# Kernel optimization log

Measured on AMD Instinct MI355X. Metric: run time of the kernel, lower is better.

The kernel has to match this reference:

```python
import jax, jax.numpy as jnp
import numpy as np
from jax import lax

L, B, N_IN, N_OUT, K = 1024, 16, 1024, 512, 5


def setup_inputs() -> dict:
    key = jax.random.key(0)
    k0, k1, k2, k3, k4 = jax.random.split(key, 5)
    val_range = (6.0 / (N_IN + N_OUT)) ** 0.5
    x = jax.random.normal(k0, (L, B, N_IN), dtype=jnp.float32)
    weight = jax.random.uniform(k1, (N_IN, N_OUT * K), dtype=jnp.float32,
                                minval=-val_range, maxval=val_range)
    bias = jax.random.normal(k2, (N_OUT * K,), dtype=jnp.float32) * 0.1
    bias_eps = jax.random.normal(k3, (N_OUT,), dtype=jnp.float32) * 0.1
    bias_final = jax.random.normal(k4, (N_OUT * 2,), dtype=jnp.float32) * 0.1
    return {"x": x, "weight": weight, "bias": bias,
            "bias_eps": bias_eps, "bias_final": bias_final}


def reference(x, weight, bias, bias_eps, bias_final):
    # x: [L, B, n_in]; unidirectional (bidir=1), real semiring, output gate, tanh
    length, batch, n_in = x.shape
    n_out = N_OUT
    u_ = (x.reshape(-1, n_in) @ weight).reshape(length, batch, n_out, K)
    b = bias.reshape(K, n_out)  # [5, n_out]: in1, in2, f1, f2, out
    forget_bias1, forget_bias2, output_bias = b[2], b[3], b[4]
    output = jax.nn.sigmoid(u_[..., 4] + output_bias)      # [L, B, n_out]
    forget1 = jax.nn.sigmoid(u_[..., 2] + forget_bias1)
    forget2 = jax.nn.sigmoid(u_[..., 3] + forget_bias2)
    u1, u2 = u_[..., 0], u_[..., 1]
    eps = jax.nn.sigmoid(bias_eps)                          # [n_out]

    def step(carry, inp):
        c1_prev, c2_prev = carry
        f1t, f2t, u1t, u2t = inp
        c1_t = c1_prev * f1t + u1t
        c2_t = c2_prev * f2t + (eps + c1_prev) * u2t
        return (c1_t, c2_t), (c1_t, c2_t)

    init = (jnp.zeros((batch, n_out), x.dtype), jnp.zeros((batch, n_out), x.dtype))
    (c1_final, c2_final), (c1s, c2s) = lax.scan(step, init, (forget1, forget2, u1, u2))

    rho = jax.nn.sigmoid(bias_final.reshape(n_out, 2)) * 2.0
    cs = c1s * rho[:, 0] + c2s * rho[:, 1]
    gcs = jnp.tanh(output * cs)                             # [L, B, n_out]
    return gcs, c1_final, c2_final
```

## Files before the change

kernel.cpp:

```cpp
#include <hip/hip_runtime.h>
#include <cstdint>

#define LSEQ 1024
#define BATCH 16
#define NIN 1024
#define NOUT 512
#define KGATE 5
#define NCOL (NOUT * KGATE)
#define MTOT (LSEQ * BATCH)
#define CHAINS (BATCH * NOUT)
#define OUT_GCS (LSEQ * BATCH * NOUT)
#define SEG 32
#define SLEN 32
#define PLANE ((size_t)MTOT * NOUT)
#define SMP ((size_t)SEG * CHAINS)

typedef _Float16 f16x8 __attribute__((ext_vector_type(8)));
typedef float f32x4 __attribute__((ext_vector_type(4)));

__device__ __forceinline__ void async16(const void* g, void* l) {
    __builtin_amdgcn_global_load_lds(
        (const __attribute__((address_space(1))) void*)(uintptr_t)g,
        (__attribute__((address_space(3))) void*)(uintptr_t)l,
        16, 0, 0);
}

__device__ __forceinline__ float fsigmoid(float x) {
    return 1.0f / (1.0f + __expf(-x));
}

__global__ void convert_x_k(const float* __restrict__ x, _Float16* __restrict__ xb, int n8) {
    int i = blockIdx.x * blockDim.x + threadIdx.x;
    if (i < n8) {
        float4 a = ((const float4*)x)[2 * i];
        float4 b = ((const float4*)x)[2 * i + 1];
        f16x8 h;
        h[0] = (_Float16)a.x; h[1] = (_Float16)a.y; h[2] = (_Float16)a.z; h[3] = (_Float16)a.w;
        h[4] = (_Float16)b.x; h[5] = (_Float16)b.y; h[6] = (_Float16)b.z; h[7] = (_Float16)b.w;
        ((f16x8*)xb)[i] = h;
    }
}

__global__ __launch_bounds__(256) void transpose_w_k(const float* __restrict__ w, _Float16* __restrict__ wT) {
    __shared__ float lds[32][33];
    int t = threadIdx.x;
    int col = t & 31;
    int rowg = t >> 5;
    int n0 = blockIdx.x * 32;
    int k0 = blockIdx.y * 32;
#pragma unroll
    for (int i = 0; i < 4; i++) {
        int r = rowg + i * 8;
        lds[r][col] = w[(size_t)(k0 + r) * NCOL + n0 + col];
    }
    __syncthreads();
#pragma unroll
    for (int i = 0; i < 4; i++) {
        int r = rowg + i * 8;
        int c = n0 + r;
        int row = (c % 5) * NOUT + (c / 5);
        wT[(size_t)row * NIN + k0 + col] = (_Float16)lds[col][r];
    }
}

__global__ __launch_bounds__(256, 2) void gemm_gates_k(const _Float16* __restrict__ A,
                                                       const _Float16* __restrict__ BT,
                                                       const float* __restrict__ bias,
                                                       _Float16* __restrict__ planes) {
    __shared__ _Float16 Al[256 * 64];
    __shared__ _Float16 Bl[128 * 64];
    int t = threadIdx.x;
    int w = t >> 6, lane = t & 63;
    int m0 = blockIdx.x * 256, n0 = blockIdx.y * 128;

    f32x4 acc[8][4] = {};

    const int q = lane >> 4, r16 = lane & 15;
    const int wm = (w >> 1) * 128, wn = (w & 1) * 64;

    for (int kk = 0; kk < NIN; kk += 64) {
#pragma unroll
        for (int cc = 0; cc < 8; cc++) {
            int c = t + cc * 256;
            int r = c >> 3, sg = c & 7;
            async16(A + (size_t)(m0 + r) * NIN + kk + sg * 8, (char*)Al + c * 16);
        }
#pragma unroll
        for (int cc = 0; cc < 4; cc++) {
            int c = t + cc * 256;
            int r = c >> 3, sg = c & 7;
            async16(BT + (size_t)(n0 + r) * NIN + kk + sg * 8, (char*)Bl + c * 16);
        }
        __syncthreads();

#pragma unroll
        for (int h = 0; h < 2; h++) {
            f16x8 af[8], bf[4];
#pragma unroll
            for (int i = 0; i < 8; i++)
                af[i] = *(const f16x8*)(Al + (wm + i * 16 + r16) * 64 + h * 32 + q * 8);
#pragma unroll
            for (int j = 0; j < 4; j++)
                bf[j] = *(const f16x8*)(Bl + (wn + j * 16 + r16) * 64 + h * 32 + q * 8);
#pragma unroll
            for (int i = 0; i < 8; i++)
#pragma unroll
                for (int j = 0; j < 4; j++)
                    acc[i][j] = __builtin_amdgcn_mfma_f32_16x16x32_f16(af[i], bf[j], acc[i][j], 0, 0, 0);
        }
        __syncthreads();
    }

    int g = n0 >> 9;
    int nb = n0 & (NOUT - 1);
    _Float16* plane = planes + (size_t)g * PLANE;
#pragma unroll
    for (int j = 0; j < 4; j++) {
        int coln = nb + wn + j * 16 + r16;
        float bv = bias[n0 + wn + j * 16 + r16];
#pragma unroll
        for (int i = 0; i < 8; i++) {
#pragma unroll
            for (int reg = 0; reg < 4; reg++) {
                int m = m0 + wm + i * 16 + q * 4 + reg;
                float v = acc[i][j][reg];
                if (g >= 2) v = fsigmoid(v + bv);
                plane[(size_t)m * NOUT + coln] = (_Float16)v;
            }
        }
    }
}

__global__ __launch_bounds__(256) void compose_k(const _Float16* __restrict__ planes,
                                                 const float* __restrict__ beps,
                                                 float* __restrict__ SM) {
    int u = blockIdx.x * 256 + threadIdx.x;
    int t = u & (CHAINS - 1);
    int s = u >> 13;
    int n = t & (NOUT - 1);
    float eps = fsigmoid(beps[n]);
    float a11 = 1.0f, a21 = 0.0f, a22 = 1.0f, b1 = 0.0f, b2 = 0.0f;
#pragma unroll 4
    for (int j = 0; j < SLEN; j++) {
        size_t e = (size_t)(s * SLEN + j) * CHAINS + t;
        float u1 = (float)planes[e];
        float u2 = (float)planes[PLANE + e];
        float f1 = (float)planes[2 * PLANE + e];
        float f2 = (float)planes[3 * PLANE + e];
        float na11 = f1 * a11;
        float na21 = fmaf(u2, a11, f2 * a21);
        float na22 = f2 * a22;
        float nb1  = fmaf(f1, b1, u1);
        float nb2  = fmaf(u2, b1, fmaf(f2, b2, eps * u2));
        a11 = na11; a21 = na21; a22 = na22; b1 = nb1; b2 = nb2;
    }
    size_t idx = (size_t)s * CHAINS + t;
    SM[idx] = a11;
    SM[SMP + idx] = a21;
    SM[2 * SMP + idx] = a22;
    SM[3 * SMP + idx] = b1;
    SM[4 * SMP + idx] = b2;
}

__global__ __launch_bounds__(256) void segscan_k(const float* __restrict__ SM,
                                                 float* __restrict__ segc,
                                                 float* __restrict__ out) {
    int t = blockIdx.x * 256 + threadIdx.x;
    float c1 = 0.0f, c2 = 0.0f;
#pragma unroll
    for (int s = 0; s < SEG; s++) {
        size_t idx = (size_t)s * CHAINS + t;
        segc[idx] = c1;
        segc[SMP + idx] = c2;
        float a11 = SM[idx];
        float a21 = SM[SMP + idx];
        float a22 = SM[2 * SMP + idx];
        float b1  = SM[3 * SMP + idx];
        float b2  = SM[4 * SMP + idx];
        float c1n = fmaf(a11, c1, b1);
        float c2n = fmaf(a21, c1, fmaf(a22, c2, b2));
        c1 = c1n; c2 = c2n;
    }
    out[OUT_GCS + t] = c1;
    out[OUT_GCS + CHAINS + t] = c2;
}

__global__ __launch_bounds__(256) void apply_k(const _Float16* __restrict__ planes,
                                               const float* __restrict__ segc,
                                               const float* __restrict__ beps,
                                               const float* __restrict__ bfin,
                                               float* __restrict__ out) {
    int u = blockIdx.x * 256 + threadIdx.x;
    int t = u & (CHAINS - 1);
    int s = u >> 13;
    int n = t & (NOUT - 1);
    float eps  = fsigmoid(beps[n]);
    float rho0 = 2.0f * fsigmoid(bfin[2 * n]);
    float rho1 = 2.0f * fsigmoid(bfin[2 * n + 1]);
    size_t idx = (size_t)s * CHAINS + t;
    float c1 = segc[idx];
    float c2 = segc[SMP + idx];
#pragma unroll 4
    for (int j = 0; j < SLEN; j++) {
        size_t e = (size_t)(s * SLEN + j) * CHAINS + t;
        float u1 = (float)planes[e];
        float u2 = (float)planes[PLANE + e];
        float f1 = (float)planes[2 * PLANE + e];
        float f2 = (float)planes[3 * PLANE + e];
        float o  = (float)planes[4 * PLANE + e];
        float c1p = c1;
        c1 = fmaf(c1p, f1, u1);
        c2 = fmaf(c2, f2, (eps + c1p) * u2);
        float cs = fmaf(c1, rho0, c2 * rho1);
        float y = o * cs;
        y = fminf(9.0f, fmaxf(-9.0f, y));
        float ex = __expf(2.0f * y);
        out[e] = (ex - 1.0f) / (ex + 1.0f);
    }
}

extern "C" void kernel_launch(void* const* d_in, const int* in_sizes, int n_in,
                              void* d_out, int out_size, void* d_ws, size_t ws_size,
                              hipStream_t stream) {
    const float* x    = (const float*)d_in[0];
    const float* wgt  = (const float*)d_in[1];
    const float* bias = (const float*)d_in[2];
    const float* beps = (const float*)d_in[3];
    const float* bfin = (const float*)d_in[4];
    float* out = (float*)d_out;

    char* p = (char*)d_ws;
    _Float16* wT     = (_Float16*)p; p += (size_t)NCOL * NIN * 2;
    _Float16* xb     = (_Float16*)p; p += (size_t)MTOT * NIN * 2;
    _Float16* planes = (_Float16*)p; p += 5 * PLANE * 2;
    float* SM        = (float*)p;    p += 5 * SMP * 4;
    float* segc      = (float*)p;    p += 2 * SMP * 4;

    transpose_w_k<<<dim3(NCOL / 32, NIN / 32), 256, 0, stream>>>(wgt, wT);

    int n8 = MTOT * NIN / 8;
    convert_x_k<<<dim3((n8 + 255) / 256), 256, 0, stream>>>(x, xb, n8);

    gemm_gates_k<<<dim3(MTOT / 256, NCOL / 128), 256, 0, stream>>>(xb, wT, bias, planes);

    compose_k<<<dim3(CHAINS * SEG / 256), 256, 0, stream>>>(planes, beps, SM);
    segscan_k<<<dim3(CHAINS / 256), 256, 0, stream>>>(SM, segc, out);
    apply_k<<<dim3(CHAINS * SEG / 256), 256, 0, stream>>>(planes, segc, beps, bfin, out);
}
```

Before: 285.8 us.

## Pipeline 256x256 gate GEMM with swizzled double-buffered LDS and vectorize scan kernels

The gate GEMM moves from a 256x128 tile with 256 threads to a 256x256 tile with 512 threads. It keeps a double-buffered, XOR-swizzled 128KB LDS tile and prefetches several K-tiles ahead with async global-to-LDS loads. The loads are interleaved with MFMA phases using explicit waitcnt, barrier and setprio control, so memory latency hides behind compute and LDS bank conflicts drop. The compose and apply kernels now process four adjacent chains per thread, using f16x4 plane loads and float4 stores to cut instruction count and widen memory accesses. The risks are lower occupancy from the large LDS footprint and subtle hand-managed synchronisation hazards.

```diff
diff --git a/kernel.cpp b/kernel.cpp
--- a/kernel.cpp
+++ b/kernel.cpp
@@ -15,7 +15,14 @@
 #define PLANE ((size_t)MTOT * NOUT)
 #define SMP ((size_t)SEG * CHAINS)
 
+#define BM 256
+#define BN 256
+#define BK 64
+#define NTILES (NIN / BK)
+#define NOBJ (4 * NTILES)
+
 typedef _Float16 f16x8 __attribute__((ext_vector_type(8)));
+typedef _Float16 f16x4 __attribute__((ext_vector_type(4)));
 typedef float f32x4 __attribute__((ext_vector_type(4)));
 
 __device__ __forceinline__ void async16(const void* g, void* l) {
@@ -63,52 +70,132 @@
     }
 }
 
-__global__ __launch_bounds__(256, 2) void gemm_gates_k(const _Float16* __restrict__ A,
+__global__ __launch_bounds__(512, 2) void gemm_gates_k(const _Float16* __restrict__ A,
                                                        const _Float16* __restrict__ BT,
                                                        const float* __restrict__ bias,
                                                        _Float16* __restrict__ planes) {
-    __shared__ _Float16 Al[256 * 64];
-    __shared__ _Float16 Bl[128 * 64];
-    int t = threadIdx.x;
-    int w = t >> 6, lane = t & 63;
-    int m0 = blockIdx.x * 256, n0 = blockIdx.y * 128;
+    __shared__ _Float16 lds[65536];
+    const int t = threadIdx.x;
+    const int w = t >> 6, lane = t & 63;
+    const int q = lane >> 4, r16 = lane & 15;
+    const int wm = (w >> 2) * 128;
+    const int wn = (w & 3) * 64;
+    const int ah = wm >> 7;
+    const int bh = wn >> 7;
+    const int wnl = wn & 127;
+    const int m0 = blockIdx.x * BM;
+    const int n0 = blockIdx.y * BN;
+
+    auto stage_obj = [&](int o) {
+        if (o >= NOBJ) return;
+        int tile = o >> 2, part = o & 3;
+        int d = tile & 1, h = part & 1;
+        _Float16* slot = lds + ((part >= 2) ? 0 : 32768) + (d * 2 + h) * 8192;
+        const _Float16* src = (part >= 2) ? (A + (size_t)(m0 + h * 128) * NIN)
+                                          : (BT + (size_t)(n0 + h * 128) * NIN);
+        int kb = tile * BK;
+#pragma unroll
+        for (int L = 0; L < 2; L++) {
+            int c = t + L * 512;
+            int r = c >> 3, kp = c & 7;
+            int k = kp ^ (r & 7);
+            async16(src + (size_t)r * NIN + kb + k * 8, (char*)lds + ((char*)slot - (char*)lds) + c * 16);
+        }
+    };
+
+    auto ldsrd = [&](const _Float16* slot, int row, int k) -> f16x8 {
+        return *(const f16x8*)(slot + row * 64 + ((k ^ (row & 7)) << 3));
+    };
 
     f32x4 acc[8][4] = {};
-
-    const int q = lane >> 4, r16 = lane & 15;
-    const int wm = (w >> 1) * 128, wn = (w & 1) * 64;
-
-    for (int kk = 0; kk < NIN; kk += 64) {
-#pragma unroll
-        for (int cc = 0; cc < 8; cc++) {
-            int c = t + cc * 256;
-            int r = c >> 3, sg = c & 7;
-            async16(A + (size_t)(m0 + r) * NIN + kk + sg * 8, (char*)Al + c * 16);
-        }
-#pragma unroll
-        for (int cc = 0; cc < 4; cc++) {
-            int c = t + cc * 256;
-            int r = c >> 3, sg = c & 7;
-            async16(BT + (size_t)(n0 + r) * NIN + kk + sg * 8, (char*)Bl + c * 16);
-        }
-        __syncthreads();
-
-#pragma unroll
-        for (int h = 0; h < 2; h++) {
-            f16x8 af[8], bf[4];
-#pragma unroll
-            for (int i = 0; i < 8; i++)
-                af[i] = *(const f16x8*)(Al + (wm + i * 16 + r16) * 64 + h * 32 + q * 8);
-#pragma unroll
-            for (int j = 0; j < 4; j++)
-                bf[j] = *(const f16x8*)(Bl + (wn + j * 16 + r16) * 64 + h * 32 + q * 8);
-#pragma unroll
-            for (int i = 0; i < 8; i++)
-#pragma unroll
-                for (int j = 0; j < 4; j++)
-                    acc[i][j] = __builtin_amdgcn_mfma_f32_16x16x32_f16(af[i], bf[j], acc[i][j], 0, 0, 0);
-        }
-        __syncthreads();
+    f16x8 a0[4][2], a1[4][2], bfr[4][2];
+
+    for (int o = 0; o < 7; o++) stage_obj(o);
+    asm volatile("s_waitcnt vmcnt(6)" ::: "memory");
+    __builtin_amdgcn_s_barrier();
+
+#pragma unroll 2
+    for (int tt = 0; tt < NTILES; tt++) {
+        const int d = tt & 1;
+        const _Float16* As = lds + (d * 2 + ah) * 8192;
+        const _Float16* Bs = lds + 32768 + (d * 2 + bh) * 8192;
+        const int ob = 4 * tt + 7;
+
+#pragma unroll
+        for (int j = 0; j < 4; j++)
+#pragma unroll
+            for (int h = 0; h < 2; h++)
+                bfr[j][h] = ldsrd(Bs, wnl + j * 16 + r16, h * 4 + q);
+#pragma unroll
+        for (int i = 0; i < 4; i++)
+#pragma unroll
+            for (int h = 0; h < 2; h++)
+                a0[i][h] = ldsrd(As, i * 16 + r16, h * 4 + q);
+        stage_obj(ob);
+        __builtin_amdgcn_s_barrier();
+        asm volatile("s_waitcnt lgkmcnt(0)" ::: "memory");
+        __builtin_amdgcn_sched_barrier(0);
+        __builtin_amdgcn_s_setprio(1);
+#pragma unroll
+        for (int i = 0; i < 4; i++)
+#pragma unroll
+            for (int j = 0; j < 2; j++)
+#pragma unroll
+                for (int h = 0; h < 2; h++)
+                    acc[i][j] = __builtin_amdgcn_mfma_f32_16x16x32_f16(a0[i][h], bfr[j][h], acc[i][j], 0, 0, 0);
+        __builtin_amdgcn_s_setprio(0);
+        __builtin_amdgcn_s_barrier();
+
+#pragma unroll
+        for (int i = 0; i < 4; i++)
+#pragma unroll
+            for (int h = 0; h < 2; h++)
+                a1[i][h] = ldsrd(As, 64 + i * 16 + r16, h * 4 + q);
+        stage_obj(ob + 1);
+        __builtin_amdgcn_s_barrier();
+        asm volatile("s_waitcnt lgkmcnt(0)" ::: "memory");
+        __builtin_amdgcn_sched_barrier(0);
+        __builtin_amdgcn_s_setprio(1);
+#pragma unroll
+        for (int i = 0; i < 4; i++)
+#pragma unroll
+            for (int j = 0; j < 2; j++)
+#pragma unroll
+                for (int h = 0; h < 2; h++)
+                    acc[4 + i][j] = __builtin_amdgcn_mfma_f32_16x16x32_f16(a1[i][h], bfr[j][h], acc[4 + i][j], 0, 0, 0);
+        __builtin_amdgcn_s_setprio(0);
+        __builtin_amdgcn_s_barrier();
+
+        stage_obj(ob + 2);
+        __builtin_amdgcn_s_barrier();
+        __builtin_amdgcn_s_setprio(1);
+#pragma unroll
+        for (int i = 0; i < 4; i++)
+#pragma unroll
+            for (int j = 0; j < 2; j++)
+#pragma unroll
+                for (int h = 0; h < 2; h++)
+                    acc[4 + i][2 + j] = __builtin_amdgcn_mfma_f32_16x16x32_f16(a1[i][h], bfr[2 + j][h], acc[4 + i][2 + j], 0, 0, 0);
+        __builtin_amdgcn_s_setprio(0);
+        __builtin_amdgcn_s_barrier();
+
+        stage_obj(ob + 3);
+        __builtin_amdgcn_s_barrier();
+        __builtin_amdgcn_s_setprio(1);
+#pragma unroll
+        for (int i = 0; i < 4; i++)
+#pragma unroll
+            for (int j = 0; j < 2; j++)
+#pragma unroll
+                for (int h = 0; h < 2; h++)
+                    acc[i][2 + j] = __builtin_amdgcn_mfma_f32_16x16x32_f16(a0[i][h], bfr[2 + j][h], acc[i][2 + j], 0, 0, 0);
+        __builtin_amdgcn_s_setprio(0);
+        if (tt < NTILES - 2) {
+            asm volatile("s_waitcnt vmcnt(6)" ::: "memory");
+        } else {
+            asm volatile("s_waitcnt vmcnt(0)" ::: "memory");
+        }
+        __builtin_amdgcn_s_barrier();
     }
 
     int g = n0 >> 9;
@@ -135,31 +222,43 @@
                                                  const float* __restrict__ beps,
                                                  float* __restrict__ SM) {
     int u = blockIdx.x * 256 + threadIdx.x;
-    int t = u & (CHAINS - 1);
-    int s = u >> 13;
-    int n = t & (NOUT - 1);
-    float eps = fsigmoid(beps[n]);
-    float a11 = 1.0f, a21 = 0.0f, a22 = 1.0f, b1 = 0.0f, b2 = 0.0f;
+    int t4 = u & (CHAINS / 4 - 1);
+    int s = u >> 11;
+    int tch = t4 << 2;
+    int n = tch & (NOUT - 1);
+    float eps[4], a11[4], a21[4], a22[4], b1[4], b2[4];
+#pragma unroll
+    for (int c = 0; c < 4; c++) {
+        eps[c] = fsigmoid(beps[n + c]);
+        a11[c] = 1.0f; a21[c] = 0.0f; a22[c] = 1.0f; b1[c] = 0.0f; b2[c] = 0.0f;
+    }
+    const f16x4* p4 = (const f16x4*)planes;
+    const size_t P4 = PLANE >> 2;
 #pragma unroll 4
     for (int j = 0; j < SLEN; j++) {
-        size_t e = (size_t)(s * SLEN + j) * CHAINS + t;
-        float u1 = (float)planes[e];
-        float u2 = (float)planes[PLANE + e];
-        float f1 = (float)planes[2 * PLANE + e];
-        float f2 = (float)planes[3 * PLANE + e];
-        float na11 = f1 * a11;
-        float na21 = fmaf(u2, a11, f2 * a21);
-        float na22 = f2 * a22;
-        float nb1  = fmaf(f1, b1, u1);
-        float nb2  = fmaf(u2, b1, fmaf(f2, b2, eps * u2));
-        a11 = na11; a21 = na21; a22 = na22; b1 = nb1; b2 = nb2;
-    }
-    size_t idx = (size_t)s * CHAINS + t;
-    SM[idx] = a11;
-    SM[SMP + idx] = a21;
-    SM[2 * SMP + idx] = a22;
-    SM[3 * SMP + idx] = b1;
-    SM[4 * SMP + idx] = b2;
+        size_t e = ((size_t)(s * SLEN + j) * CHAINS + tch) >> 2;
+        f16x4 u1v = p4[e];
+        f16x4 u2v = p4[P4 + e];
+        f16x4 f1v = p4[2 * P4 + e];
+        f16x4 f2v = p4[3 * P4 + e];
+#pragma unroll
+        for (int c = 0; c < 4; c++) {
+            float u1 = (float)u1v[c], u2 = (float)u2v[c];
+            float f1 = (float)f1v[c], f2 = (float)f2v[c];
+            float na11 = f1 * a11[c];
+            float na21 = fmaf(u2, a11[c], f2 * a21[c]);
+            float na22 = f2 * a22[c];
+            float nb1  = fmaf(f1, b1[c], u1);
+            float nb2  = fmaf(u2, b1[c], fmaf(f2, b2[c], eps[c] * u2));
+            a11[c] = na11; a21[c] = na21; a22[c] = na22; b1[c] = nb1; b2[c] = nb2;
+        }
+    }
+    size_t idx = (size_t)s * CHAINS + tch;
+    *(float4*)(SM + idx)           = make_float4(a11[0], a11[1], a11[2], a11[3]);
+    *(float4*)(SM + SMP + idx)     = make_float4(a21[0], a21[1], a21[2], a21[3]);
+    *(float4*)(SM + 2 * SMP + idx) = make_float4(a22[0], a22[1], a22[2], a22[3]);
+    *(float4*)(SM + 3 * SMP + idx) = make_float4(b1[0], b1[1], b1[2], b1[3]);
+    *(float4*)(SM + 4 * SMP + idx) = make_float4(b2[0], b2[1], b2[2], b2[3]);
 }
 
 __global__ __launch_bounds__(256) void segscan_k(const float* __restrict__ SM,
@@ -191,31 +290,51 @@
                                                const float* __restrict__ bfin,
                                                float* __restrict__ out) {
     int u = blockIdx.x * 256 + threadIdx.x;
-    int t = u & (CHAINS - 1);
-    int s = u >> 13;
-    int n = t & (NOUT - 1);
-    float eps  = fsigmoid(beps[n]);
-    float rho0 = 2.0f * fsigmoid(bfin[2 * n]);
-    float rho1 = 2.0f * fsigmoid(bfin[2 * n + 1]);
-    size_t idx = (size_t)s * CHAINS + t;
-    float c1 = segc[idx];
-    float c2 = segc[SMP + idx];
+    int t4 = u & (CHAINS / 4 - 1);
+    int s = u >> 11;
+    int tch = t4 << 2;
+    int n = tch & (NOUT - 1);
+    float eps[4], rho0[4], rho1[4], c1[4], c2[4];
+#pragma unroll
+    for (int c = 0; c < 4; c++) {
+        eps[c]  = fsigmoid(beps[n + c]);
+        rho0[c] = 2.0f * fsigmoid(bfin[2 * (n + c)]);
+        rho1[c] = 2.0f * fsigmoid(bfin[2 * (n + c) + 1]);
+    }
+    size_t idx = (size_t)s * CHAINS + tch;
+    float4 c1v = *(const float4*)(segc + idx);
+    float4 c2v = *(const float4*)(segc + SMP + idx);
+    c1[0] = c1v.x; c1[1] = c1v.y; c1[2] = c1v.z; c1[3] = c1v.w;
+    c2[0] = c2v.x; c2[1] = c2v.y; c2[2] = c2v.z; c2[3] = c2v.w;
+    const f16x4* p4 = (const f16x4*)planes;
+    const size_t P4 = PLANE >> 2;
 #pragma unroll 4
     for (int j = 0; j < SLEN; j++) {
-        size_t e = (size_t)(s * SLEN + j) * CHAINS + t;
-        float u1 = (float)planes[e];
-        float u2 = (float)planes[PLANE + e];
-        float f1 = (float)planes[2 * PLANE + e];
-        float f2 = (float)planes[3 * PLANE + e];
-        float o  = (float)planes[4 * PLANE + e];
-        float c1p = c1;
-        c1 = fmaf(c1p, f1, u1);
-        c2 = fmaf(c2, f2, (eps + c1p) * u2);
-        float cs = fmaf(c1, rho0, c2 * rho1);
-        float y = o * cs;
-        y = fminf(9.0f, fmaxf(-9.0f, y));
-        float ex = __expf(2.0f * y);
-        out[e] = (ex - 1.0f) / (ex + 1.0f);
+        size_t e = (size_t)(s * SLEN + j) * CHAINS + tch;
+        size_t e4 = e >> 2;
+        f16x4 u1v = p4[e4];
+        f16x4 u2v = p4[P4 + e4];
+        f16x4 f1v = p4[2 * P4 + e4];
+        f16x4 f2v = p4[3 * P4 + e4];
+        f16x4 ov  = p4[4 * P4 + e4];
+        float4 yv;
+        float yr[4];
+#pragma unroll
+        for (int c = 0; c < 4; c++) {
+            float u1 = (float)u1v[c], u2 = (float)u2v[c];
+            float f1 = (float)f1v[c], f2 = (float)f2v[c];
+            float o  = (float)ov[c];
+            float c1p = c1[c];
+            c1[c] = fmaf(c1p, f1, u1);
+            c2[c] = fmaf(c2[c], f2, (eps[c] + c1p) * u2);
+            float cs = fmaf(c1[c], rho0[c], c2[c] * rho1[c]);
+            float y = o * cs;
+            y = fminf(9.0f, fmaxf(-9.0f, y));
+            float ex = __expf(2.0f * y);
+            yr[c] = (ex - 1.0f) / (ex + 1.0f);
+        }
+        yv.x = yr[0]; yv.y = yr[1]; yv.z = yr[2]; yv.w = yr[3];
+        *(float4*)(out + e) = yv;
     }
 }
 
@@ -241,9 +360,9 @@
     int n8 = MTOT * NIN / 8;
     convert_x_k<<<dim3((n8 + 255) / 256), 256, 0, stream>>>(x, xb, n8);
 
-    gemm_gates_k<<<dim3(MTOT / 256, NCOL / 128), 256, 0, stream>>>(xb, wT, bias, planes);
-
-    compose_k<<<dim3(CHAINS * SEG / 256), 256, 0, stream>>>(planes, beps, SM);
+    gemm_gates_k<<<dim3(MTOT / BM, NCOL / BN), 512, 0, stream>>>(xb, wT, bias, planes);
+
+    compose_k<<<dim3(SEG * CHAINS / 4 / 256), 256, 0, stream>>>(planes, beps, SM);
     segscan_k<<<dim3(CHAINS / 256), 256, 0, stream>>>(SM, segc, out);
-    apply_k<<<dim3(CHAINS * SEG / 256), 256, 0, stream>>>(planes, segc, beps, bfin, out);
-}
+    apply_k<<<dim3(SEG * CHAINS / 4 / 256), 256, 0, stream>>>(planes, segc, beps, bfin, out);
+}
```

After: 299.1 us. 1.05x slower.
